# Optimization experiments

Measured on AMD Instinct MI355X. Metric: run time of the kernel, lower is better.

## Reference

```python
import jax, jax.numpy as jnp
import numpy as np

B = 1048576
EPS = 1e-5

def _lin_params(key, din, dout):
    k1, k2 = jax.random.split(key)
    bound = 1.0 / np.sqrt(din)
    w = jax.random.uniform(k1, (din, dout), minval=-bound, maxval=bound, dtype=jnp.float32)
    b = jax.random.uniform(k2, (dout,), minval=-bound, maxval=bound, dtype=jnp.float32)
    return w, b

def setup_inputs() -> dict:
    key = jax.random.key(0)
    ks = jax.random.split(key, 10)
    x = jax.random.normal(ks[0], (B, 8), dtype=jnp.float32)
    dims = [(8, 16), (16, 16), (16, 12), (12, 8), (8, 4), (4, 4), (4, 4), (4, 1)]
    names = ['fm', 'c1', 'p1', 'c2', 'p2', 'c3', 'r', 'h']
    inp = {'x': x,
           'bn_g': jnp.ones((8,), jnp.float32),
           'bn_b': jnp.zeros((8,), jnp.float32)}
    for i, (nm, (di, do)) in enumerate(zip(names, dims)):
        w, b = _lin_params(ks[i + 1], di, do)
        inp['w_' + nm] = w
        inp['b_' + nm] = b
    return inp

def reference(x, bn_g, bn_b, w_fm, b_fm, w_c1, b_c1, w_p1, b_p1, w_c2, b_c2,
              w_p2, b_p2, w_c3, b_c3, w_r, b_r, w_h, b_h):
    # BatchNorm1d (training mode): batch statistics, biased variance
    mu = jnp.mean(x, axis=0)
    var = jnp.mean((x - mu) ** 2, axis=0)
    h = (x - mu) * jax.lax.rsqrt(var + EPS) * bn_g + bn_b
    h = jnp.tanh(h @ w_fm + b_fm)   # [B,16] feature_map
    h = jnp.tanh(h @ w_c1 + b_c1)   # [B,16] conv1
    h = jnp.tanh(h @ w_p1 + b_p1)   # [B,12] pool1
    h = jnp.tanh(h @ w_c2 + b_c2)   # [B,8]  conv2
    h = jnp.tanh(h @ w_p2 + b_p2)   # [B,4]  pool2
    h = jnp.tanh(h @ w_c3 + b_c3)   # [B,4]  conv3
    res = jax.nn.relu(h @ w_r + b_r)  # [B,4] residual branch
    h = h + res
    return jax.nn.sigmoid(h @ w_h + b_h)  # [B,1]
```

## Files before the change

kernel.cpp:

```cpp
#include <hip/hip_runtime.h>
#include <stdint.h>

#define B_ROWS 1048576

typedef __fp16 h2 __attribute__((ext_vector_type(2)));

#define WPK_OFF 16
#define BIA_OFF 386
#define W_FM 0
#define W_C1 64
#define W_P1 192
#define W_C2 288
#define W_P2 336
#define W_C3 352
#define W_R  360
#define W_H  368
#define B_FM 0
#define B_C1 16
#define B_P1 32
#define B_C2 44
#define B_P2 52
#define B_C3 56
#define B_R  60
#define B_H  64

__device__ __forceinline__ float fast_tanh(float x) {
    float e = __builtin_amdgcn_exp2f(x * 2.8853900817779268f);
    return 1.0f - 2.0f * __builtin_amdgcn_rcpf(e + 1.0f);
}

__device__ __forceinline__ float fast_sigmoid(float x) {
    float e = __builtin_amdgcn_exp2f(x * -1.4426950408889634f);
    return __builtin_amdgcn_rcpf(1.0f + e);
}

__global__ __launch_bounds__(256) void bn_stats(const float* __restrict__ x,
                                                float* __restrict__ ws) {
    const int tid = blockIdx.x * 256 + threadIdx.x;
    float s[8], q[8];
#pragma unroll
    for (int c = 0; c < 8; ++c) { s[c] = 0.f; q[c] = 0.f; }
    const float4* x4 = (const float4*)x;
#pragma unroll
    for (int k = 0; k < 4; ++k) {
        int r = tid + k * 262144;
        float4 a = x4[2 * r];
        float4 b = x4[2 * r + 1];
        s[0] += a.x; s[1] += a.y; s[2] += a.z; s[3] += a.w;
        s[4] += b.x; s[5] += b.y; s[6] += b.z; s[7] += b.w;
        q[0] += a.x * a.x; q[1] += a.y * a.y; q[2] += a.z * a.z; q[3] += a.w * a.w;
        q[4] += b.x * b.x; q[5] += b.y * b.y; q[6] += b.z * b.z; q[7] += b.w * b.w;
    }
#pragma unroll
    for (int off = 32; off > 0; off >>= 1) {
#pragma unroll
        for (int c = 0; c < 8; ++c) {
            s[c] += __shfl_down(s[c], off);
            q[c] += __shfl_down(q[c], off);
        }
    }
    __shared__ float red[4][16];
    const int lane = threadIdx.x & 63;
    const int wave = threadIdx.x >> 6;
    if (lane == 0) {
#pragma unroll
        for (int c = 0; c < 8; ++c) { red[wave][c] = s[c]; red[wave][8 + c] = q[c]; }
    }
    __syncthreads();
    if (threadIdx.x < 16) {
        float acc = red[0][threadIdx.x] + red[1][threadIdx.x] +
                    red[2][threadIdx.x] + red[3][threadIdx.x];
        atomicAdd(&ws[threadIdx.x], acc);
    }
}

template<int DIN, int DOUT>
__device__ void pack_layer(const float* __restrict__ w, const float* __restrict__ b,
                           uint32_t* __restrict__ wdst, float* __restrict__ bdst,
                           const float* sc, const float* sh, bool fold) {
    for (int idx = threadIdx.x; idx < DOUT * (DIN / 2); idx += blockDim.x) {
        int j = idx / (DIN / 2), i2 = idx % (DIN / 2);
        float w0 = w[(2 * i2) * DOUT + j];
        float w1 = w[(2 * i2 + 1) * DOUT + j];
        if (fold) { w0 *= sc[2 * i2]; w1 *= sc[2 * i2 + 1]; }
        h2 h; h.x = (__fp16)w0; h.y = (__fp16)w1;
        wdst[j * (DIN / 2) + i2] = __builtin_bit_cast(uint32_t, h);
    }
    for (int j = threadIdx.x; j < DOUT; j += blockDim.x) {
        float bb = b[j];
        if (fold) {
#pragma unroll
            for (int i = 0; i < 8; ++i) bb += sh[i] * w[i * DOUT + j];
        }
        bdst[j] = bb;
    }
}

__global__ __launch_bounds__(256) void prep(
    float* __restrict__ ws,
    const float* __restrict__ bn_g, const float* __restrict__ bn_b,
    const float* __restrict__ w_fm, const float* __restrict__ b_fm,
    const float* __restrict__ w_c1, const float* __restrict__ b_c1,
    const float* __restrict__ w_p1, const float* __restrict__ b_p1,
    const float* __restrict__ w_c2, const float* __restrict__ b_c2,
    const float* __restrict__ w_p2, const float* __restrict__ b_p2,
    const float* __restrict__ w_c3, const float* __restrict__ b_c3,
    const float* __restrict__ w_r,  const float* __restrict__ b_r,
    const float* __restrict__ w_h,  const float* __restrict__ b_h)
{
    const float invB = 1.0f / (float)B_ROWS;
    float sc[8], sh[8];
#pragma unroll
    for (int c = 0; c < 8; ++c) {
        float mu  = ws[c] * invB;
        float var = fmaf(-mu, mu, ws[8 + c] * invB);
        float s   = bn_g[c] * rsqrtf(var + 1e-5f);
        sc[c] = s;
        sh[c] = fmaf(-mu, s, bn_b[c]);
    }
    uint32_t* wpk = (uint32_t*)(ws + WPK_OFF);
    float*    bpk = ws + BIA_OFF;
    pack_layer<8, 16>(w_fm, b_fm, wpk + W_FM, bpk + B_FM, sc, sh, true);
    pack_layer<16,16>(w_c1, b_c1, wpk + W_C1, bpk + B_C1, sc, sh, false);
    pack_layer<16,12>(w_p1, b_p1, wpk + W_P1, bpk + B_P1, sc, sh, false);
    pack_layer<12, 8>(w_c2, b_c2, wpk + W_C2, bpk + B_C2, sc, sh, false);
    pack_layer<8,  4>(w_p2, b_p2, wpk + W_P2, bpk + B_P2, sc, sh, false);
    pack_layer<4,  4>(w_c3, b_c3, wpk + W_C3, bpk + B_C3, sc, sh, false);
    pack_layer<4,  4>(w_r,  b_r,  wpk + W_R,  bpk + B_R,  sc, sh, false);
    pack_layer<4,  1>(w_h,  b_h,  wpk + W_H,  bpk + B_H,  sc, sh, false);
}

template<int DIN, int DOUT>
__device__ __forceinline__ void layer_dot(const h2* __restrict__ apk, float* __restrict__ out,
                                          const uint32_t* __restrict__ wpk,
                                          const float* __restrict__ bias) {
#pragma unroll
    for (int j = 0; j < DOUT; ++j) {
        float acc = bias[j];
#pragma unroll
        for (int i2 = 0; i2 < DIN / 2; ++i2) {
            h2 w = __builtin_bit_cast(h2, wpk[j * (DIN / 2) + i2]);
            acc = __builtin_amdgcn_fdot2(apk[i2], w, acc, false);
        }
        out[j] = acc;
    }
}

template<int N>
__device__ __forceinline__ void tanh_pack(const float* __restrict__ in, h2* __restrict__ apk) {
#pragma unroll
    for (int k = 0; k < N / 2; ++k) {
        float t0 = fast_tanh(in[2 * k]);
        float t1 = fast_tanh(in[2 * k + 1]);
        apk[k] = __builtin_amdgcn_cvt_pkrtz(t0, t1);
    }
}

__global__ __launch_bounds__(256) void qcnn_main(
    const float* __restrict__ x,
    const float* __restrict__ ws, float* __restrict__ out)
{
    const uint32_t* wpk = (const uint32_t*)(ws + WPK_OFF);
    const float*    bpk = ws + BIA_OFF;

    const int tid = blockIdx.x * 256 + threadIdx.x;
    const float4* x4 = (const float4*)x;
    float4 xa = x4[2 * tid], xb = x4[2 * tid + 1];

    h2 a8[4];
    a8[0] = __builtin_amdgcn_cvt_pkrtz(xa.x, xa.y);
    a8[1] = __builtin_amdgcn_cvt_pkrtz(xa.z, xa.w);
    a8[2] = __builtin_amdgcn_cvt_pkrtz(xb.x, xb.y);
    a8[3] = __builtin_amdgcn_cvt_pkrtz(xb.z, xb.w);

    float o16[16]; h2 p16[8];
    layer_dot<8, 16>(a8, o16, wpk + W_FM, bpk + B_FM);  tanh_pack<16>(o16, p16);
    float o16b[16]; h2 p16b[8];
    layer_dot<16,16>(p16, o16b, wpk + W_C1, bpk + B_C1); tanh_pack<16>(o16b, p16b);
    float o12[12]; h2 p12[6];
    layer_dot<16,12>(p16b, o12, wpk + W_P1, bpk + B_P1); tanh_pack<12>(o12, p12);
    float o8[8]; h2 p8[4];
    layer_dot<12, 8>(p12, o8, wpk + W_C2, bpk + B_C2);   tanh_pack<8>(o8, p8);
    float o4[4]; h2 p4[2];
    layer_dot<8,  4>(p8, o4, wpk + W_P2, bpk + B_P2);    tanh_pack<4>(o4, p4);
    float c4[4];
    layer_dot<4,  4>(p4, c4, wpk + W_C3, bpk + B_C3);
#pragma unroll
    for (int j = 0; j < 4; ++j) c4[j] = fast_tanh(c4[j]);
    h2 pc4[2];
    pc4[0] = __builtin_amdgcn_cvt_pkrtz(c4[0], c4[1]);
    pc4[1] = __builtin_amdgcn_cvt_pkrtz(c4[2], c4[3]);
    float r4[4];
    layer_dot<4,  4>(pc4, r4, wpk + W_R, bpk + B_R);
#pragma unroll
    for (int j = 0; j < 4; ++j) c4[j] += fmaxf(r4[j], 0.f);
    h2 ph[2];
    ph[0] = __builtin_amdgcn_cvt_pkrtz(c4[0], c4[1]);
    ph[1] = __builtin_amdgcn_cvt_pkrtz(c4[2], c4[3]);
    float oh[1];
    layer_dot<4,  1>(ph, oh, wpk + W_H, bpk + B_H);
    out[tid] = fast_sigmoid(oh[0]);
}

extern "C" void kernel_launch(void* const* d_in, const int* in_sizes, int n_in,
                              void* d_out, int out_size, void* d_ws, size_t ws_size,
                              hipStream_t stream) {
    const float* x    = (const float*)d_in[0];
    const float* bn_g = (const float*)d_in[1];
    const float* bn_b = (const float*)d_in[2];
    const float* w_fm = (const float*)d_in[3];
    const float* b_fm = (const float*)d_in[4];
    const float* w_c1 = (const float*)d_in[5];
    const float* b_c1 = (const float*)d_in[6];
    const float* w_p1 = (const float*)d_in[7];
    const float* b_p1 = (const float*)d_in[8];
    const float* w_c2 = (const float*)d_in[9];
    const float* b_c2 = (const float*)d_in[10];
    const float* w_p2 = (const float*)d_in[11];
    const float* b_p2 = (const float*)d_in[12];
    const float* w_c3 = (const float*)d_in[13];
    const float* b_c3 = (const float*)d_in[14];
    const float* w_r  = (const float*)d_in[15];
    const float* b_r  = (const float*)d_in[16];
    const float* w_h  = (const float*)d_in[17];
    const float* b_h  = (const float*)d_in[18];
    float* out = (float*)d_out;
    float* ws  = (float*)d_ws;

    (void)hipMemsetAsync(d_ws, 0, 16 * sizeof(float), stream);
    bn_stats<<<1024, 256, 0, stream>>>(x, ws);
    prep<<<1, 256, 0, stream>>>(ws, bn_g, bn_b, w_fm, b_fm, w_c1, b_c1, w_p1, b_p1,
                                w_c2, b_c2, w_p2, b_p2, w_c3, b_c3, w_r, b_r, w_h, b_h);
    qcnn_main<<<B_ROWS / 256, 256, 0, stream>>>(x, ws, out);
}
```

Before: 155.3 us.

## Replace exp-based tanh with shared-memory LUT and process two rows per thread

```diff
diff --git a/kernel.cpp b/kernel.cpp
--- a/kernel.cpp
+++ b/kernel.cpp
@@ -2,6 +2,8 @@
 #include <stdint.h>
 
 #define B_ROWS 1048576
+#define ROWS_PER_THREAD 2
+#define MAIN_BLOCKS (B_ROWS / (256 * ROWS_PER_THREAD))
 
 typedef __fp16 h2 __attribute__((ext_vector_type(2)));
 
@@ -24,7 +26,7 @@
 #define B_R  60
 #define B_H  64
 
-__device__ __forceinline__ float fast_tanh(float x) {
+__device__ __forceinline__ float exp_tanh(float x) {
     float e = __builtin_amdgcn_exp2f(x * 2.8853900817779268f);
     return 1.0f - 2.0f * __builtin_amdgcn_rcpf(e + 1.0f);
 }
@@ -130,29 +132,47 @@
     pack_layer<4,  1>(w_h,  b_h,  wpk + W_H,  bpk + B_H,  sc, sh, false);
 }
 
+__device__ __forceinline__ float lut_tanh(float x, const float2* __restrict__ lut) {
+    float t  = fmaf(x, 128.0f, 512.0f);
+    t = __builtin_amdgcn_fmed3f(t, 0.0f, 1023.998f);
+    float fl = floorf(t);
+    float fr = t - fl;
+    float2 e = lut[(int)fl];
+    return fmaf(e.y, fr, e.x);
+}
+
 template<int DIN, int DOUT>
-__device__ __forceinline__ void layer_dot(const h2* __restrict__ apk, float* __restrict__ out,
+__device__ __forceinline__ void layer_dot(const h2* __restrict__ apkA, const h2* __restrict__ apkB,
+                                          float* __restrict__ outA, float* __restrict__ outB,
                                           const uint32_t* __restrict__ wpk,
                                           const float* __restrict__ bias) {
 #pragma unroll
     for (int j = 0; j < DOUT; ++j) {
-        float acc = bias[j];
+        float accA = bias[j];
+        float accB = accA;
 #pragma unroll
         for (int i2 = 0; i2 < DIN / 2; ++i2) {
             h2 w = __builtin_bit_cast(h2, wpk[j * (DIN / 2) + i2]);
-            acc = __builtin_amdgcn_fdot2(apk[i2], w, acc, false);
-        }
-        out[j] = acc;
+            accA = __builtin_amdgcn_fdot2(apkA[i2], w, accA, false);
+            accB = __builtin_amdgcn_fdot2(apkB[i2], w, accB, false);
+        }
+        outA[j] = accA;
+        outB[j] = accB;
     }
 }
 
 template<int N>
-__device__ __forceinline__ void tanh_pack(const float* __restrict__ in, h2* __restrict__ apk) {
+__device__ __forceinline__ void tanh_pack(const float* __restrict__ inA, const float* __restrict__ inB,
+                                          h2* __restrict__ pkA, h2* __restrict__ pkB,
+                                          const float2* __restrict__ lut) {
 #pragma unroll
     for (int k = 0; k < N / 2; ++k) {
-        float t0 = fast_tanh(in[2 * k]);
-        float t1 = fast_tanh(in[2 * k + 1]);
-        apk[k] = __builtin_amdgcn_cvt_pkrtz(t0, t1);
+        float a0 = lut_tanh(inA[2 * k], lut);
+        float a1 = lut_tanh(inA[2 * k + 1], lut);
+        float b0 = lut_tanh(inB[2 * k], lut);
+        float b1 = lut_tanh(inB[2 * k + 1], lut);
+        pkA[k] = __builtin_amdgcn_cvt_pkrtz(a0, a1);
+        pkB[k] = __builtin_amdgcn_cvt_pkrtz(b0, b1);
     }
 }
 
@@ -160,46 +180,82 @@
     const float* __restrict__ x,
     const float* __restrict__ ws, float* __restrict__ out)
 {
+    __shared__ float2 lut[1024];
+    {
+        const float h = 0.0078125f;
+#pragma unroll
+        for (int k = 0; k < 4; ++k) {
+            int i = threadIdx.x + k * 256;
+            float x0 = fmaf((float)i, h, -4.0f);
+            float t0 = exp_tanh(x0);
+            float t1 = exp_tanh(x0 + h);
+            lut[i] = make_float2(t0, t1 - t0);
+        }
+    }
+    __syncthreads();
+
     const uint32_t* wpk = (const uint32_t*)(ws + WPK_OFF);
     const float*    bpk = ws + BIA_OFF;
 
     const int tid = blockIdx.x * 256 + threadIdx.x;
+    const int r0 = tid, r1 = tid + (B_ROWS / 2);
     const float4* x4 = (const float4*)x;
-    float4 xa = x4[2 * tid], xb = x4[2 * tid + 1];
-
-    h2 a8[4];
-    a8[0] = __builtin_amdgcn_cvt_pkrtz(xa.x, xa.y);
-    a8[1] = __builtin_amdgcn_cvt_pkrtz(xa.z, xa.w);
-    a8[2] = __builtin_amdgcn_cvt_pkrtz(xb.x, xb.y);
-    a8[3] = __builtin_amdgcn_cvt_pkrtz(xb.z, xb.w);
-
-    float o16[16]; h2 p16[8];
-    layer_dot<8, 16>(a8, o16, wpk + W_FM, bpk + B_FM);  tanh_pack<16>(o16, p16);
-    float o16b[16]; h2 p16b[8];
-    layer_dot<16,16>(p16, o16b, wpk + W_C1, bpk + B_C1); tanh_pack<16>(o16b, p16b);
-    float o12[12]; h2 p12[6];
-    layer_dot<16,12>(p16b, o12, wpk + W_P1, bpk + B_P1); tanh_pack<12>(o12, p12);
-    float o8[8]; h2 p8[4];
-    layer_dot<12, 8>(p12, o8, wpk + W_C2, bpk + B_C2);   tanh_pack<8>(o8, p8);
-    float o4[4]; h2 p4[2];
-    layer_dot<8,  4>(p8, o4, wpk + W_P2, bpk + B_P2);    tanh_pack<4>(o4, p4);
-    float c4[4];
-    layer_dot<4,  4>(p4, c4, wpk + W_C3, bpk + B_C3);
-#pragma unroll
-    for (int j = 0; j < 4; ++j) c4[j] = fast_tanh(c4[j]);
-    h2 pc4[2];
-    pc4[0] = __builtin_amdgcn_cvt_pkrtz(c4[0], c4[1]);
-    pc4[1] = __builtin_amdgcn_cvt_pkrtz(c4[2], c4[3]);
-    float r4[4];
-    layer_dot<4,  4>(pc4, r4, wpk + W_R, bpk + B_R);
-#pragma unroll
-    for (int j = 0; j < 4; ++j) c4[j] += fmaxf(r4[j], 0.f);
-    h2 ph[2];
-    ph[0] = __builtin_amdgcn_cvt_pkrtz(c4[0], c4[1]);
-    ph[1] = __builtin_amdgcn_cvt_pkrtz(c4[2], c4[3]);
-    float oh[1];
-    layer_dot<4,  1>(ph, oh, wpk + W_H, bpk + B_H);
-    out[tid] = fast_sigmoid(oh[0]);
+    float4 xa0 = x4[2 * r0], xa1 = x4[2 * r0 + 1];
+    float4 xb0 = x4[2 * r1], xb1 = x4[2 * r1 + 1];
+
+    h2 a8[4], b8[4];
+    a8[0] = __builtin_amdgcn_cvt_pkrtz(xa0.x, xa0.y);
+    a8[1] = __builtin_amdgcn_cvt_pkrtz(xa0.z, xa0.w);
+    a8[2] = __builtin_amdgcn_cvt_pkrtz(xa1.x, xa1.y);
+    a8[3] = __builtin_amdgcn_cvt_pkrtz(xa1.z, xa1.w);
+    b8[0] = __builtin_amdgcn_cvt_pkrtz(xb0.x, xb0.y);
+    b8[1] = __builtin_amdgcn_cvt_pkrtz(xb0.z, xb0.w);
+    b8[2] = __builtin_amdgcn_cvt_pkrtz(xb1.x, xb1.y);
+    b8[3] = __builtin_amdgcn_cvt_pkrtz(xb1.z, xb1.w);
+
+    float oA[16], oB[16]; h2 pA[8], pB[8];
+    layer_dot<8, 16>(a8, b8, oA, oB, wpk + W_FM, bpk + B_FM);
+    tanh_pack<16>(oA, oB, pA, pB, lut);
+    float o2A[16], o2B[16]; h2 p2A[8], p2B[8];
+    layer_dot<16,16>(pA, pB, o2A, o2B, wpk + W_C1, bpk + B_C1);
+    tanh_pack<16>(o2A, o2B, p2A, p2B, lut);
+    float o3A[12], o3B[12]; h2 p3A[6], p3B[6];
+    layer_dot<16,12>(p2A, p2B, o3A, o3B, wpk + W_P1, bpk + B_P1);
+    tanh_pack<12>(o3A, o3B, p3A, p3B, lut);
+    float o4A[8], o4B[8]; h2 p4A[4], p4B[4];
+    layer_dot<12, 8>(p3A, p3B, o4A, o4B, wpk + W_C2, bpk + B_C2);
+    tanh_pack<8>(o4A, o4B, p4A, p4B, lut);
+    float o5A[4], o5B[4]; h2 p5A[2], p5B[2];
+    layer_dot<8,  4>(p4A, p4B, o5A, o5B, wpk + W_P2, bpk + B_P2);
+    tanh_pack<4>(o5A, o5B, p5A, p5B, lut);
+    float c4A[4], c4B[4];
+    layer_dot<4,  4>(p5A, p5B, c4A, c4B, wpk + W_C3, bpk + B_C3);
+#pragma unroll
+    for (int j = 0; j < 4; ++j) {
+        c4A[j] = lut_tanh(c4A[j], lut);
+        c4B[j] = lut_tanh(c4B[j], lut);
+    }
+    h2 pcA[2], pcB[2];
+    pcA[0] = __builtin_amdgcn_cvt_pkrtz(c4A[0], c4A[1]);
+    pcA[1] = __builtin_amdgcn_cvt_pkrtz(c4A[2], c4A[3]);
+    pcB[0] = __builtin_amdgcn_cvt_pkrtz(c4B[0], c4B[1]);
+    pcB[1] = __builtin_amdgcn_cvt_pkrtz(c4B[2], c4B[3]);
+    float r4A[4], r4B[4];
+    layer_dot<4,  4>(pcA, pcB, r4A, r4B, wpk + W_R, bpk + B_R);
+#pragma unroll
+    for (int j = 0; j < 4; ++j) {
+        c4A[j] += fmaxf(r4A[j], 0.f);
+        c4B[j] += fmaxf(r4B[j], 0.f);
+    }
+    h2 phA[2], phB[2];
+    phA[0] = __builtin_amdgcn_cvt_pkrtz(c4A[0], c4A[1]);
+    phA[1] = __builtin_amdgcn_cvt_pkrtz(c4A[2], c4A[3]);
+    phB[0] = __builtin_amdgcn_cvt_pkrtz(c4B[0], c4B[1]);
+    phB[1] = __builtin_amdgcn_cvt_pkrtz(c4B[2], c4B[3]);
+    float ohA[1], ohB[1];
+    layer_dot<4,  1>(phA, phB, ohA, ohB, wpk + W_H, bpk + B_H);
+    out[r0] = fast_sigmoid(ohA[0]);
+    out[r1] = fast_sigmoid(ohB[0]);
 }
 
 extern "C" void kernel_launch(void* const* d_in, const int* in_sizes, int n_in,
@@ -231,5 +287,5 @@
     bn_stats<<<1024, 256, 0, stream>>>(x, ws);
     prep<<<1, 256, 0, stream>>>(ws, bn_g, bn_b, w_fm, b_fm, w_c1, b_c1, w_p1, b_p1,
                                 w_c2, b_c2, w_p2, b_p2, w_c3, b_c3, w_r, b_r, w_h, b_h);
-    qcnn_main<<<B_ROWS / 256, 256, 0, stream>>>(x, ws, out);
-}
+    qcnn_main<<<MAIN_BLOCKS, 256, 0, stream>>>(x, ws, out);
+}
```

Result: no change. 153.3 us (-1.2%).
